# Kernel tuning notes

Hardware: AMD Instinct MI355X
Metric: run time of the kernel (lower is better)

## Reference

```python
import math
import jax, jax.numpy as jnp
import numpy as np

B, N, D = 8, 1024, 1024


def setup_inputs() -> dict:
    key = jax.random.key(0)
    ks = jax.random.split(key, 5)
    scale = 1.0 / math.sqrt(D)  # ~torch Linear init scale
    x = jax.random.normal(ks[0], (B, N, D), jnp.float32)
    Wq = jax.random.uniform(ks[1], (D, D), jnp.float32, -scale, scale)
    Wk = jax.random.uniform(ks[2], (D, D), jnp.float32, -scale, scale)
    Wv = jax.random.uniform(ks[3], (D, D), jnp.float32, -scale, scale)
    Ws = jax.random.uniform(ks[4], (D, 1), jnp.float32, -scale, scale)
    return {"x": x, "Wq": Wq, "Wk": Wk, "Wv": Wv, "Ws": Ws}


def reference(x, Wq, Wk, Wv, Ws):
    # projections
    Q = x @ Wq                      # [B, N, D]
    K = x @ Wk
    V = x @ Wv
    sigma = x @ Ws                  # [B, N, 1]
    sigma = jax.nn.sigmoid(sigma * 5.0) + 1e-5
    sigma = jnp.power(3.0, sigma) - 1.0

    # prior association: Gaussian kernel over |i-j| distances
    idx = jnp.arange(N, dtype=jnp.float32)
    dist = jnp.abs(idx[:, None] - idx[None, :])            # [N, N]
    inv_norm = 1.0 / (jnp.sqrt(2.0 * jnp.pi) * sigma)      # [B, N, 1]
    gaussian = inv_norm * jnp.exp(-0.5 * jnp.square(dist / sigma))  # [B, N, N]
    P = gaussian / gaussian.sum(axis=(1, 2), keepdims=True)

    # series association: softmax over the BATCH dim (dim=0), as in source
    scores = jnp.einsum('bnd,bmd->bnm', Q, K) / math.sqrt(D)  # [B, N, N]
    S = jax.nn.softmax(scores, axis=0)

    # reconstruction
    Z = jnp.einsum('bnm,bmd->bnd', S, V)                     # [B, N, D]
    return Z, P
```

## Files before the change

### kernel.cpp

```cpp
#include <hip/hip_runtime.h>
#include <hip/hip_fp16.h>


typedef __attribute__((ext_vector_type(8))) short bf16x8;
typedef __attribute__((ext_vector_type(4))) float f32x4;
typedef unsigned short ushort_t;

#define DI __device__ __forceinline__

constexpr long NN = 1024L * 1024L;
constexpr long ND = 1024L * 1024L;

DI ushort_t f2bf(float f) {
    unsigned int u = __float_as_uint(f);
    u = u + 0x7fffu + ((u >> 16) & 1u);
    return (ushort_t)(u >> 16);
}
DI ushort_t f2h(float f) {
    __half h = __float2half(f);
    return *(ushort_t*)&h;
}
DI float h2f(ushort_t u) {
    __half h = *(__half*)&u;
    return __half2float(h);
}

template <int OUT_BF16>
DI void g3b_body(const ushort_t* __restrict__ Ab, const ushort_t* __restrict__ Bb,
                 void* __restrict__ Cb, int ldA, int ldB, int ldC,
                 float scale, int bx, int by, ushort_t* lds)
{
    constexpr int BUF   = 24576;
    constexpr int B_OFF = 8192;

    const int tid  = threadIdx.x;
    const int wave = tid >> 6;
    const int lane = tid & 63;
    const int wm   = wave >> 2;
    const int wn   = wave & 3;
    const int gm   = bx * 128;
    const int gn   = by * 256;

    const int srow = tid >> 3;
    const int scol = 8 * ((tid & 7) ^ (srow & 7));
    const int sdst = wave * 512;

    auto stageA = [&](int t, int d, int h) {
        const ushort_t* src = Ab + (long)(gm + h * 64 + srow) * ldA + t * 64 + scol;
        __builtin_amdgcn_global_load_lds(
            (const __attribute__((address_space(1))) void*)src,
            (__attribute__((address_space(3))) void*)(&lds[d * BUF + h * 4096 + sdst]),
            16, 0, 0);
    };
    auto stageB = [&](int t, int d, int h, int j) {
        const ushort_t* src = Bb + (long)(gn + h * 128 + j * 64 + srow) * ldB + t * 64 + scol;
        __builtin_amdgcn_global_load_lds(
            (const __attribute__((address_space(1))) void*)src,
            (__attribute__((address_space(3))) void*)(&lds[d * BUF + B_OFF + h * 8192 + j * 4096 + sdst]),
            16, 0, 0);
    };

    const int arow = wm * 64 + (lane & 15);
    const int brow = wn * 64 + (lane & 15);
    const int cs0 = (((lane >> 4) * 16) ^ ((lane & 7) << 4)) >> 1;
    const int cs1 = ((64 + (lane >> 4) * 16) ^ ((lane & 7) << 4)) >> 1;

    f32x4 acc[4][4];
#pragma unroll
    for (int m = 0; m < 4; ++m)
#pragma unroll
        for (int n = 0; n < 4; ++n) acc[m][n] = (f32x4){0.f, 0.f, 0.f, 0.f};

    stageA(0, 0, 0); stageA(0, 0, 1);
    stageB(0, 0, 0, 0); stageB(0, 0, 0, 1); stageB(0, 0, 1, 0); stageB(0, 0, 1, 1);
    stageA(1, 1, 0); stageA(1, 1, 1);
    stageB(1, 1, 0, 0); stageB(1, 1, 0, 1); stageB(1, 1, 1, 0); stageB(1, 1, 1, 1);
    asm volatile("s_waitcnt vmcnt(6)" ::: "memory");
    __builtin_amdgcn_s_barrier();
    __builtin_amdgcn_sched_barrier(0);

    int cur = 0;
    for (int t = 0; t < 16; ++t) {
        const int nxt = (cur == 0) ? 2 : cur - 1;
        const ushort_t* la = &lds[cur * BUF];
        const ushort_t* lb = &lds[cur * BUF + B_OFF];

        bf16x8 a[2][4], b[2][4];
#pragma unroll
        for (int mi = 0; mi < 4; ++mi) {
            a[0][mi] = *(const bf16x8*)&la[(arow + mi * 16) * 64 + cs0];
            a[1][mi] = *(const bf16x8*)&la[(arow + mi * 16) * 64 + cs1];
        }
#pragma unroll
        for (int ni = 0; ni < 2; ++ni) {
            b[0][ni] = *(const bf16x8*)&lb[(brow + ni * 16) * 64 + cs0];
            b[1][ni] = *(const bf16x8*)&lb[(brow + ni * 16) * 64 + cs1];
        }
        if (t < 14) {
            stageB(t + 2, nxt, 0, 0); stageB(t + 2, nxt, 0, 1);
            stageB(t + 2, nxt, 1, 0); stageB(t + 2, nxt, 1, 1);
        }
        __builtin_amdgcn_s_barrier();
        asm volatile("s_waitcnt lgkmcnt(0)" ::: "memory");
        __builtin_amdgcn_sched_barrier(0);
        __builtin_amdgcn_s_setprio(1);
#pragma unroll
        for (int mi = 0; mi < 4; ++mi)
#pragma unroll
            for (int ni = 0; ni < 2; ++ni) {
                acc[mi][ni] = __builtin_amdgcn_mfma_f32_16x16x32_bf16(a[0][mi], b[0][ni], acc[mi][ni], 0, 0, 0);
                acc[mi][ni] = __builtin_amdgcn_mfma_f32_16x16x32_bf16(a[1][mi], b[1][ni], acc[mi][ni], 0, 0, 0);
            }
        __builtin_amdgcn_s_setprio(0);
        __builtin_amdgcn_s_barrier();
        __builtin_amdgcn_sched_barrier(0);

#pragma unroll
        for (int ni = 2; ni < 4; ++ni) {
            b[0][ni] = *(const bf16x8*)&lb[(brow + ni * 16) * 64 + cs0];
            b[1][ni] = *(const bf16x8*)&lb[(brow + ni * 16) * 64 + cs1];
        }
        if (t < 14) { stageA(t + 2, nxt, 0); stageA(t + 2, nxt, 1); }
        __builtin_amdgcn_s_barrier();
        asm volatile("s_waitcnt lgkmcnt(0)" ::: "memory");
        if (t < 14) asm volatile("s_waitcnt vmcnt(6)" ::: "memory");
        else        asm volatile("s_waitcnt vmcnt(0)" ::: "memory");
        __builtin_amdgcn_sched_barrier(0);
        __builtin_amdgcn_s_setprio(1);
#pragma unroll
        for (int mi = 0; mi < 4; ++mi)
#pragma unroll
            for (int ni = 2; ni < 4; ++ni) {
                acc[mi][ni] = __builtin_amdgcn_mfma_f32_16x16x32_bf16(a[0][mi], b[0][ni], acc[mi][ni], 0, 0, 0);
                acc[mi][ni] = __builtin_amdgcn_mfma_f32_16x16x32_bf16(a[1][mi], b[1][ni], acc[mi][ni], 0, 0, 0);
            }
        __builtin_amdgcn_s_setprio(0);
        __builtin_amdgcn_s_barrier();
        __builtin_amdgcn_sched_barrier(0);

        cur = (cur == 2) ? 0 : cur + 1;
    }

    if (OUT_BF16) {
        ushort_t* el = lds;
#pragma unroll
        for (int mi = 0; mi < 4; ++mi)
#pragma unroll
            for (int ni = 0; ni < 4; ++ni)
#pragma unroll
                for (int r = 0; r < 4; ++r)
                    el[(wm * 64 + mi * 16 + (lane >> 4) * 4 + r) * 256 +
                       wn * 64 + ni * 16 + (lane & 15)] = f2bf(acc[mi][ni][r] * scale);
        __builtin_amdgcn_s_barrier();
        ushort_t* C = (ushort_t*)Cb;
#pragma unroll
        for (int rr = 0; rr < 8; ++rr) {
            const int row = rr * 16 + (tid >> 5);
            const int col = (tid & 31) * 8;
            *(bf16x8*)&C[(long)(gm + row) * ldC + gn + col] =
                *(const bf16x8*)&el[row * 256 + col];
        }
    } else {
        float* el = (float*)lds;
        float* C  = (float*)Cb;
#pragma unroll
        for (int h = 0; h < 2; ++h) {
            if (wm == h) {
#pragma unroll
                for (int mi = 0; mi < 4; ++mi)
#pragma unroll
                    for (int ni = 0; ni < 4; ++ni)
#pragma unroll
                        for (int r = 0; r < 4; ++r)
                            el[(mi * 16 + (lane >> 4) * 4 + r) * 256 +
                               wn * 64 + ni * 16 + (lane & 15)] = acc[mi][ni][r] * scale;
            }
            __builtin_amdgcn_s_barrier();
#pragma unroll
            for (int i = 0; i < 8; ++i) {
                const int cc  = i * 512 + tid;
                const int row = cc >> 6;
                const int c4  = (cc & 63) * 4;
                *(float4*)&C[(long)(gm + h * 64 + row) * ldC + gn + c4] =
                    *(const float4*)&el[row * 256 + c4];
            }
            __builtin_amdgcn_s_barrier();
        }
    }
}

template <int OUT_BF16>
__global__ __launch_bounds__(512, 2)
void gemm3b(const ushort_t* __restrict__ A, const ushort_t* __restrict__ B,
            void* __restrict__ Cout, int ldA, int ldB, int ldC,
            long sA, long sB, long sC, float scale,
            int n0, int n1, int xfirst)
{
    __shared__ ushort_t lds[3 * 24576];
    const int total = gridDim.x;
    const int lin   = blockIdx.x;
    const int swz   = (lin & 7) * (total >> 3) + (lin >> 3);
    const int c0    = swz % n0;
    const int rem   = swz / n0;
    const int c1    = rem % n1;
    const int bz    = rem / n1;
    const int bx    = xfirst ? c0 : c1;
    const int by    = xfirst ? c1 : c0;
    void* Cb = OUT_BF16 ? (void*)((ushort_t*)Cout + (long)bz * sC)
                        : (void*)((float*)Cout + (long)bz * sC);
    g3b_body<OUT_BF16>(A + (long)bz * sA, B + (long)bz * sB, Cb,
                       ldA, ldB, ldC, scale, bx, by, lds);
}

template <int OUT_MODE>
DI void g256_body(const ushort_t* __restrict__ Ab, const ushort_t* __restrict__ Bb,
                  void* __restrict__ Cb, int ldA, int ldB, int ldC,
                  float scale, int bx, int by, ushort_t* ldsp)
{
    constexpr int BUF   = 32768;
    constexpr int B_OFF = 16384;

    const int tid  = threadIdx.x;
    const int wave = tid >> 6;
    const int lane = tid & 63;
    const int wm   = wave >> 2;
    const int wn   = wave & 3;
    const int gm   = bx * 256;
    const int gn   = by * 256;

    const int srow = tid >> 3;
    const int scol = 8 * ((tid & 7) ^ (srow & 7));
    const int sdst = wave * 512;

    auto stage = [&](int t, int d, int op, int h) {
        const ushort_t* g  = op ? Bb : Ab;
        const int       ld = op ? ldB : ldA;
        const int       g0 = (op ? gn : gm) + h * 128;
#pragma unroll
        for (int j = 0; j < 2; ++j) {
            const ushort_t* src = g + (long)(g0 + j * 64 + srow) * ld + t * 64 + scol;
            __builtin_amdgcn_global_load_lds(
                (const __attribute__((address_space(1))) void*)src,
                (__attribute__((address_space(3))) void*)
                    (&ldsp[d * BUF + op * B_OFF + h * 8192 + j * 4096 + sdst]),
                16, 0, 0);
        }
    };

    const int arow = wm * 128 + (lane & 15);
    const int brow = wn * 64 + (lane & 15);
    const int cs0 = (((lane >> 4) * 16) ^ ((lane & 7) << 4)) >> 1;
    const int cs1 = ((64 + (lane >> 4) * 16) ^ ((lane & 7) << 4)) >> 1;

    f32x4 acc[8][4];
#pragma unroll
    for (int m = 0; m < 8; ++m)
#pragma unroll
        for (int n = 0; n < 4; ++n) acc[m][n] = (f32x4){0.f, 0.f, 0.f, 0.f};

    stage(0, 0, 0, 0); stage(0, 0, 0, 1); stage(0, 0, 1, 0); stage(0, 0, 1, 1);
    stage(1, 1, 0, 0); stage(1, 1, 0, 1); stage(1, 1, 1, 0); stage(1, 1, 1, 1);
    asm volatile("s_waitcnt vmcnt(8)" ::: "memory");
    __builtin_amdgcn_s_barrier();
    __builtin_amdgcn_sched_barrier(0);

    bf16x8 a[2][4], b0[2][2], b1[2][2];
#pragma unroll 2
    for (int t = 0; t < 16; ++t) {
        const int cur = t & 1;
        const ushort_t* la = &ldsp[cur * BUF];
        const ushort_t* lb = &ldsp[cur * BUF + B_OFF];

#pragma unroll
        for (int mi = 0; mi < 4; ++mi) {
            a[0][mi] = *(const bf16x8*)&la[(arow + mi * 16) * 64 + cs0];
            a[1][mi] = *(const bf16x8*)&la[(arow + mi * 16) * 64 + cs1];
        }
#pragma unroll
        for (int ni = 0; ni < 2; ++ni) {
            b0[0][ni] = *(const bf16x8*)&lb[(brow + ni * 16) * 64 + cs0];
            b0[1][ni] = *(const bf16x8*)&lb[(brow + ni * 16) * 64 + cs1];
        }
        __builtin_amdgcn_s_barrier();
        asm volatile("s_waitcnt lgkmcnt(0)" ::: "memory");
        __builtin_amdgcn_sched_barrier(0);
        __builtin_amdgcn_s_setprio(1);
#pragma unroll
        for (int mi = 0; mi < 4; ++mi)
#pragma unroll
            for (int ni = 0; ni < 2; ++ni) {
                acc[mi][ni] = __builtin_amdgcn_mfma_f32_16x16x32_bf16(a[0][mi], b0[0][ni], acc[mi][ni], 0, 0, 0);
                acc[mi][ni] = __builtin_amdgcn_mfma_f32_16x16x32_bf16(a[1][mi], b0[1][ni], acc[mi][ni], 0, 0, 0);
            }
        __builtin_amdgcn_s_setprio(0);
        __builtin_amdgcn_s_barrier();
        __builtin_amdgcn_sched_barrier(0);

#pragma unroll
        for (int ni = 0; ni < 2; ++ni) {
            b1[0][ni] = *(const bf16x8*)&lb[(brow + (ni + 2) * 16) * 64 + cs0];
            b1[1][ni] = *(const bf16x8*)&lb[(brow + (ni + 2) * 16) * 64 + cs1];
        }
        __builtin_amdgcn_s_barrier();
        asm volatile("s_waitcnt lgkmcnt(0)" ::: "memory");
        __builtin_amdgcn_sched_barrier(0);
        __builtin_amdgcn_s_setprio(1);
#pragma unroll
        for (int mi = 0; mi < 4; ++mi)
#pragma unroll
            for (int ni = 0; ni < 2; ++ni) {
                acc[mi][ni + 2] = __builtin_amdgcn_mfma_f32_16x16x32_bf16(a[0][mi], b1[0][ni], acc[mi][ni + 2], 0, 0, 0);
                acc[mi][ni + 2] = __builtin_amdgcn_mfma_f32_16x16x32_bf16(a[1][mi], b1[1][ni], acc[mi][ni + 2], 0, 0, 0);
            }
        __builtin_amdgcn_s_setprio(0);
        __builtin_amdgcn_s_barrier();
        __builtin_amdgcn_sched_barrier(0);

#pragma unroll
        for (int mi = 0; mi < 4; ++mi) {
            a[0][mi] = *(const bf16x8*)&la[(arow + (mi + 4) * 16) * 64 + cs0];
            a[1][mi] = *(const bf16x8*)&la[(arow + (mi + 4) * 16) * 64 + cs1];
        }
        if (t < 14) { stage(t + 2, cur, 1, 0); stage(t + 2, cur, 1, 1); }
        __builtin_amdgcn_s_barrier();
        asm volatile("s_waitcnt lgkmcnt(0)" ::: "memory");
        __builtin_amdgcn_sched_barrier(0);
        __builtin_amdgcn_s_setprio(1);
#pragma unroll
        for (int mi = 0; mi < 4; ++mi)
#pragma unroll
            for (int ni = 0; ni < 2; ++ni) {
                acc[mi + 4][ni + 2] = __builtin_amdgcn_mfma_f32_16x16x32_bf16(a[0][mi], b1[0][ni], acc[mi + 4][ni + 2], 0, 0, 0);
                acc[mi + 4][ni + 2] = __builtin_amdgcn_mfma_f32_16x16x32_bf16(a[1][mi], b1[1][ni], acc[mi + 4][ni + 2], 0, 0, 0);
            }
        __builtin_amdgcn_s_setprio(0);
        __builtin_amdgcn_s_barrier();
        __builtin_amdgcn_sched_barrier(0);

        if (t < 14) { stage(t + 2, cur, 0, 0); stage(t + 2, cur, 0, 1); }
        if (t < 14)       asm volatile("s_waitcnt vmcnt(8)" ::: "memory");
        else if (t == 14) asm volatile("s_waitcnt vmcnt(0)" ::: "memory");
        __builtin_amdgcn_sched_barrier(0);
        __builtin_amdgcn_s_setprio(1);
#pragma unroll
        for (int mi = 0; mi < 4; ++mi)
#pragma unroll
            for (int ni = 0; ni < 2; ++ni) {
                acc[mi + 4][ni] = __builtin_amdgcn_mfma_f32_16x16x32_bf16(a[0][mi], b0[0][ni], acc[mi + 4][ni], 0, 0, 0);
                acc[mi + 4][ni] = __builtin_amdgcn_mfma_f32_16x16x32_bf16(a[1][mi], b0[1][ni], acc[mi + 4][ni], 0, 0, 0);
            }
        __builtin_amdgcn_s_setprio(0);
        __builtin_amdgcn_s_barrier();
        __builtin_amdgcn_sched_barrier(0);
    }

    if (OUT_MODE != 0) {
        ushort_t* el = ldsp;
#pragma unroll
        for (int mi = 0; mi < 8; ++mi)
#pragma unroll
            for (int ni = 0; ni < 4; ++ni)
#pragma unroll
                for (int r = 0; r < 4; ++r) {
                    const float v = acc[mi][ni][r] * scale;
                    el[(wm * 128 + mi * 16 + (lane >> 4) * 4 + r) * 256 +
                       wn * 64 + ni * 16 + (lane & 15)] =
                        (OUT_MODE == 1) ? f2bf(v) : f2h(v);
                }
        __builtin_amdgcn_s_barrier();
        ushort_t* C = (ushort_t*)Cb;
#pragma unroll
        for (int i = 0; i < 16; ++i) {
            const int cc  = i * 512 + tid;
            const int row = cc >> 5;
            const int col = (cc & 31) * 8;
            *(bf16x8*)&C[(long)(gm + row) * ldC + gn + col] =
                *(const bf16x8*)&el[row * 256 + col];
        }
    } else {
        float* el = (float*)ldsp;
        float* C  = (float*)Cb;
#pragma unroll
        for (int h = 0; h < 2; ++h) {
            if (wm == h) {
#pragma unroll
                for (int mi = 0; mi < 8; ++mi)
#pragma unroll
                    for (int ni = 0; ni < 4; ++ni)
#pragma unroll
                        for (int r = 0; r < 4; ++r)
                            el[(mi * 16 + (lane >> 4) * 4 + r) * 256 +
                               wn * 64 + ni * 16 + (lane & 15)] = acc[mi][ni][r] * scale;
            }
            __builtin_amdgcn_s_barrier();
#pragma unroll
            for (int i = 0; i < 16; ++i) {
                const int cc  = i * 512 + tid;
                const int row = cc >> 6;
                const int c4  = (cc & 63) * 4;
                *(float4*)&C[(long)(gm + h * 128 + row) * ldC + gn + c4] =
                    *(const float4*)&el[row * 256 + c4];
            }
            __builtin_amdgcn_s_barrier();
        }
    }
}

__global__ __launch_bounds__(512)
void prep_g(const float* __restrict__ x, const float* __restrict__ Ws,
            const float* __restrict__ Wq, const float* __restrict__ Wk,
            const float* __restrict__ Wv,
            ushort_t* __restrict__ xh, float* __restrict__ sigma,
            float* __restrict__ rowsum,
            ushort_t* __restrict__ WvT, ushort_t* __restrict__ G)
{
    __shared__ char smem[20608];
    const int blk = blockIdx.x;
    const int tid = threadIdx.x;

    if (blk < 160) {
        const int wave = tid >> 6, lane = tid & 63;
        for (int row = blk * 8 + wave; row < 8192; row += 1280) {
            const float* xr = x + (long)row * 1024;
            float dot = 0.f;
#pragma unroll
            for (int c = 0; c < 4; ++c) {
                const int i = c * 256 + lane * 4;
                float4 v = *(const float4*)(xr + i);
                float4 w = *(const float4*)(Ws + i);
                dot += v.x * w.x + v.y * w.y + v.z * w.z + v.w * w.w;
                ushort4 o;
                o.x = f2bf(v.x); o.y = f2bf(v.y); o.z = f2bf(v.z); o.w = f2bf(v.w);
                *(ushort4*)(xh + (long)row * 1024 + i) = o;
            }
#pragma unroll
            for (int o = 32; o; o >>= 1) dot += __shfl_down(dot, o);
            float sg;
            if (lane == 0) {
                float s = 1.f / (1.f + __expf(-5.f * dot)) + 1e-5f;
                sg = exp2f(s * 1.5849625007211562f) - 1.f;
            }
            sg = __shfl(sg, 0);
            const int i = row & 1023;
            const float c = -0.5f / (sg * sg);
            float a = 0.f;
            for (int j = lane; j < 1024; j += 64) {
                float d = (float)(i - j);
                a += __expf(c * d * d);
            }
#pragma unroll
            for (int o = 32; o; o >>= 1) a += __shfl_down(a, o);
            if (lane == 0) {
                sigma[row]  = sg;
                rowsum[row] = (0.3989422804014327f / sg) * a;
            }
        }
    } else if (blk < 192) {
        float (*s)[65] = (float(*)[65])smem;
        const int r = tid >> 4, c4 = (tid & 15) * 4;
#pragma unroll
        for (int it = 0; it < 8; ++it) {
            const int tile = (blk - 160) * 8 + it;
            const int tr = (tile >> 4) * 64, tc = (tile & 15) * 64;
#pragma unroll
            for (int rr = r; rr < 64; rr += 32) {
                float4 v = *(const float4*)(Wv + (long)(tr + rr) * 1024 + tc + c4);
                s[rr][c4] = v.x; s[rr][c4 + 1] = v.y; s[rr][c4 + 2] = v.z; s[rr][c4 + 3] = v.w;
            }
            __syncthreads();
#pragma unroll
            for (int rr = r; rr < 64; rr += 32) {
                ushort4 o;
                o.x = f2bf(s[c4][rr]);     o.y = f2bf(s[c4 + 1][rr]);
                o.z = f2bf(s[c4 + 2][rr]); o.w = f2bf(s[c4 + 3][rr]);
                *(ushort4*)(WvT + (long)(tc + rr) * 1024 + tr + c4) = o;
            }
            __syncthreads();
        }
    } else {
        ushort_t* sA = (ushort_t*)smem;
        ushort_t* sB = sA + 5120;
        const int g  = blk - 192;
        const int gm = (g >> 3) * 128, gn = (g & 7) * 128;
        const int wave = tid >> 6, lane = tid & 63;
        const int wm = wave >> 2, wn = wave & 3;
        const int lrow = tid >> 3, lcol = (tid & 7) * 4;
        const float* A0 = Wk + (long)(gm + lrow) * 1024 + lcol;
        const float* A1 = Wk + (long)(gm + 64 + lrow) * 1024 + lcol;
        const float* B0 = Wq + (long)(gn + lrow) * 1024 + lcol;
        const float* B1 = Wq + (long)(gn + 64 + lrow) * 1024 + lcol;

        f32x4 acc[4][2];
#pragma unroll
        for (int m = 0; m < 4; ++m)
#pragma unroll
            for (int n = 0; n < 2; ++n) acc[m][n] = (f32x4){0.f, 0.f, 0.f, 0.f};

        auto wr = [&](float4 a0, float4 a1, float4 b0, float4 b1) {
            ushort4 o;
            o.x = f2bf(a0.x); o.y = f2bf(a0.y); o.z = f2bf(a0.z); o.w = f2bf(a0.w);
            *(ushort4*)&sA[lrow * 40 + lcol] = o;
            o.x = f2bf(a1.x); o.y = f2bf(a1.y); o.z = f2bf(a1.z); o.w = f2bf(a1.w);
            *(ushort4*)&sA[(64 + lrow) * 40 + lcol] = o;
            o.x = f2bf(b0.x); o.y = f2bf(b0.y); o.z = f2bf(b0.z); o.w = f2bf(b0.w);
            *(ushort4*)&sB[lrow * 40 + lcol] = o;
            o.x = f2bf(b1.x); o.y = f2bf(b1.y); o.z = f2bf(b1.z); o.w = f2bf(b1.w);
            *(ushort4*)&sB[(64 + lrow) * 40 + lcol] = o;
        };
        auto mm = [&]() {
            bf16x8 af[4], bfv[2];
#pragma unroll
            for (int mi = 0; mi < 4; ++mi)
                af[mi] = *(const bf16x8*)&sA[(wm * 64 + mi * 16 + (lane & 15)) * 40 + (lane >> 4) * 8];
#pragma unroll
            for (int ni = 0; ni < 2; ++ni)
                bfv[ni] = *(const bf16x8*)&sB[(wn * 32 + ni * 16 + (lane & 15)) * 40 + (lane >> 4) * 8];
#pragma unroll
            for (int mi = 0; mi < 4; ++mi)
#pragma unroll
                for (int ni = 0; ni < 2; ++ni)
                    acc[mi][ni] = __builtin_amdgcn_mfma_f32_16x16x32_bf16(af[mi], bfv[ni], acc[mi][ni], 0, 0, 0);
        };

        float4 a0A = *(const float4*)(A0);      float4 a1A = *(const float4*)(A1);
        float4 b0A = *(const float4*)(B0);      float4 b1A = *(const float4*)(B1);
        float4 a0B = *(const float4*)(A0 + 32); float4 a1B = *(const float4*)(A1 + 32);
        float4 b0B = *(const float4*)(B0 + 32); float4 b1B = *(const float4*)(B1 + 32);

        for (int k0 = 0; k0 < 1024; k0 += 64) {
            wr(a0A, a1A, b0A, b1A);
            if (k0 < 960) {
                a0A = *(const float4*)(A0 + k0 + 64); a1A = *(const float4*)(A1 + k0 + 64);
                b0A = *(const float4*)(B0 + k0 + 64); b1A = *(const float4*)(B1 + k0 + 64);
            }
            __syncthreads();
            mm();
            __syncthreads();
            wr(a0B, a1B, b0B, b1B);
            if (k0 < 928) {
                a0B = *(const float4*)(A0 + k0 + 96); a1B = *(const float4*)(A1 + k0 + 96);
                b0B = *(const float4*)(B0 + k0 + 96); b1B = *(const float4*)(B1 + k0 + 96);
            }
            __syncthreads();
            mm();
            __syncthreads();
        }
#pragma unroll
        for (int mi = 0; mi < 4; ++mi)
#pragma unroll
            for (int ni = 0; ni < 2; ++ni)
#pragma unroll
                for (int r = 0; r < 4; ++r)
                    G[(long)(gm + wm * 64 + mi * 16 + (lane >> 4) * 4 + r) * 1024 +
                      gn + wn * 32 + ni * 16 + (lane & 15)] = f2bf(acc[mi][ni][r]);
    }
}

__global__ __launch_bounds__(512, 2)
void sc_vt(const ushort_t* __restrict__ xqh, const ushort_t* __restrict__ xh,
           ushort_t* __restrict__ scoresH,
           const ushort_t* __restrict__ WvT, ushort_t* __restrict__ VTall)
{
    __shared__ ushort_t lds[2 * 32768];
    const int lin = blockIdx.x;
    if (lin < 128) {
        const int bz = lin & 7;
        const int t  = lin >> 3;
        g256_body<2>(xqh + (long)bz * ND, xh + (long)bz * ND,
                     (void*)(scoresH + (long)bz * NN),
                     1024, 1024, 1024, 0.03125f, t & 3, t >> 2, lds);
    } else {
        const int l  = lin - 128;
        const int l2 = (l & 7) * 16 + (l >> 3);
        g256_body<1>(WvT, xh, (void*)VTall,
                     1024, 1024, 8192, 1.f, l2 & 3, l2 >> 2, lds);
    }
}

__global__ __launch_bounds__(256)
void softmax_prior(const ushort_t* __restrict__ scoresH, ushort_t* __restrict__ S,
                   const float* __restrict__ sigma, const float* __restrict__ rowsum,
                   float* __restrict__ P)
{
    __shared__ float sred[256];
    const int blk = blockIdx.x;
    const int tid = threadIdx.x;
    if (blk < 4096) {
        const long idx = (long)blk * 256 + tid;
        float v[8], m = -1e30f;
#pragma unroll
        for (int b = 0; b < 8; ++b) { v[b] = h2f(scoresH[(long)b * NN + idx]); m = fmaxf(m, v[b]); }
        float sum = 0.f;
#pragma unroll
        for (int b = 0; b < 8; ++b) { v[b] = __expf(v[b] - m); sum += v[b]; }
        const float inv = 1.f / sum;
#pragma unroll
        for (int b = 0; b < 8; ++b) S[(long)b * NN + idx] = f2bf(v[b] * inv);
    } else {
        const int l = blk - 4096;
        const int b = l >> 7;
        float a = rowsum[b * 1024 + tid]       + rowsum[b * 1024 + 256 + tid] +
                  rowsum[b * 1024 + 512 + tid] + rowsum[b * 1024 + 768 + tid];
        sred[tid] = a; __syncthreads();
        for (int o = 128; o; o >>= 1) { if (tid < o) sred[tid] += sred[tid + o]; __syncthreads(); }
        const float bs = sred[0];
        const int r0 = (l & 127) * 8;
#pragma unroll
        for (int it = 0; it < 8; ++it) {
            const int e   = it * 256 + tid;
            const int row = r0 + (e >> 8);
            const int j4  = (e & 255) * 4;
            const float sg  = sigma[(b << 10) + row];
            const float c   = -0.5f / (sg * sg);
            const float inv = 0.3989422804014327f / (sg * bs);
            float4 o;
            float d;
            d = (float)(row - j4);       o.x = inv * __expf(c * d * d);
            d = (float)(row - j4 - 1);   o.y = inv * __expf(c * d * d);
            d = (float)(row - j4 - 2);   o.z = inv * __expf(c * d * d);
            d = (float)(row - j4 - 3);   o.w = inv * __expf(c * d * d);
            *(float4*)&P[(long)b * NN + (long)row * 1024 + j4] = o;
        }
    }
}

extern "C" void kernel_launch(void* const* d_in, const int* in_sizes, int n_in,
                              void* d_out, int out_size, void* d_ws, size_t ws_size,
                              hipStream_t stream)
{
    const float* x  = (const float*)d_in[0];
    const float* Wq = (const float*)d_in[1];
    const float* Wk = (const float*)d_in[2];
    const float* Wv = (const float*)d_in[3];
    const float* Ws = (const float*)d_in[4];
    float* Zout = (float*)d_out;
    float* Pout = Zout + 8 * ND;

    char* base = (char*)d_ws;
    size_t off = 0;
    auto alloc = [&](size_t bytes) {
        void* p = base + off;
        off = (off + bytes + 255) & ~(size_t)255;
        return p;
    };
    ushort_t* xh      = (ushort_t*)alloc(8192L * 1024 * 2);
    ushort_t* G       = (ushort_t*)alloc(NN * 2);
    ushort_t* WvT     = (ushort_t*)alloc(NN * 2);
    ushort_t* xqh     = (ushort_t*)alloc(8192L * 1024 * 2);
    ushort_t* VTall   = (ushort_t*)alloc(1024L * 8192 * 2);
    ushort_t* scoresH = (ushort_t*)alloc(8L * NN * 2);
    float* sigma      = (float*)alloc(8192 * 4);
    float* rowsum     = (float*)alloc(8192 * 4);
    ushort_t* Sh      = xh;

    prep_g<<<256, 512, 0, stream>>>(x, Ws, Wq, Wk, Wv, xh, sigma, rowsum, WvT, G);
    gemm3b<1><<<256, 512, 0, stream>>>(
        xh, G, xqh, 1024, 1024, 1024, 0, 0, 0, 1.f, 4, 64, 0);
    sc_vt<<<256, 512, 0, stream>>>(xqh, xh, scoresH, WvT, VTall);
    softmax_prior<<<5120, 256, 0, stream>>>(scoresH, Sh, sigma, rowsum, Pout);
    gemm3b<0><<<256, 512, 0, stream>>>(
        Sh, VTall, Zout, 1024, 8192, 1024, NN, 1024, ND, 1.f, 8, 4, 1);
}
```

Before: 118.9 us.

## Shrink GEMM tile to 128x128 with double-buffered LDS and more blocks

Replaces the 128x256 triple-buffered GEMM with a 128x128 tile, two LDS buffers, and a unified stage helper. Grid size doubles to 512 blocks and launch bounds allow four blocks per CU. The aim is better occupancy and CU fill for the two 1024-wide GEMMs. The cost is less operand reuse per block, so more global and LDS traffic per FLOP, plus a shallower prefetch pipeline.

```diff
diff --git a/kernel.cpp b/kernel.cpp
--- a/kernel.cpp
+++ b/kernel.cpp
@@ -26,11 +26,11 @@
 }
 
 template <int OUT_BF16>
-DI void g3b_body(const ushort_t* __restrict__ Ab, const ushort_t* __restrict__ Bb,
+DI void g2b_body(const ushort_t* __restrict__ Ab, const ushort_t* __restrict__ Bb,
                  void* __restrict__ Cb, int ldA, int ldB, int ldC,
                  float scale, int bx, int by, ushort_t* lds)
 {
-    constexpr int BUF   = 24576;
+    constexpr int BUF   = 16384;
     constexpr int B_OFF = 8192;
 
     const int tid  = threadIdx.x;
@@ -39,53 +39,48 @@
     const int wm   = wave >> 2;
     const int wn   = wave & 3;
     const int gm   = bx * 128;
-    const int gn   = by * 256;
+    const int gn   = by * 128;
 
     const int srow = tid >> 3;
     const int scol = 8 * ((tid & 7) ^ (srow & 7));
     const int sdst = wave * 512;
 
-    auto stageA = [&](int t, int d, int h) {
-        const ushort_t* src = Ab + (long)(gm + h * 64 + srow) * ldA + t * 64 + scol;
+    auto stage = [&](int t, int d, int op, int h) {
+        const ushort_t* g  = op ? Bb : Ab;
+        const int       ld = op ? ldB : ldA;
+        const int       g0 = (op ? gn : gm) + h * 64;
+        const ushort_t* src = g + (long)(g0 + srow) * ld + t * 64 + scol;
         __builtin_amdgcn_global_load_lds(
             (const __attribute__((address_space(1))) void*)src,
-            (__attribute__((address_space(3))) void*)(&lds[d * BUF + h * 4096 + sdst]),
+            (__attribute__((address_space(3))) void*)
+                (&lds[d * BUF + op * B_OFF + h * 4096 + sdst]),
             16, 0, 0);
     };
-    auto stageB = [&](int t, int d, int h, int j) {
-        const ushort_t* src = Bb + (long)(gn + h * 128 + j * 64 + srow) * ldB + t * 64 + scol;
-        __builtin_amdgcn_global_load_lds(
-            (const __attribute__((address_space(1))) void*)src,
-            (__attribute__((address_space(3))) void*)(&lds[d * BUF + B_OFF + h * 8192 + j * 4096 + sdst]),
-            16, 0, 0);
-    };
 
     const int arow = wm * 64 + (lane & 15);
-    const int brow = wn * 64 + (lane & 15);
+    const int brow = wn * 32 + (lane & 15);
     const int cs0 = (((lane >> 4) * 16) ^ ((lane & 7) << 4)) >> 1;
     const int cs1 = ((64 + (lane >> 4) * 16) ^ ((lane & 7) << 4)) >> 1;
 
-    f32x4 acc[4][4];
+    f32x4 acc[4][2];
 #pragma unroll
     for (int m = 0; m < 4; ++m)
 #pragma unroll
-        for (int n = 0; n < 4; ++n) acc[m][n] = (f32x4){0.f, 0.f, 0.f, 0.f};
-
-    stageA(0, 0, 0); stageA(0, 0, 1);
-    stageB(0, 0, 0, 0); stageB(0, 0, 0, 1); stageB(0, 0, 1, 0); stageB(0, 0, 1, 1);
-    stageA(1, 1, 0); stageA(1, 1, 1);
-    stageB(1, 1, 0, 0); stageB(1, 1, 0, 1); stageB(1, 1, 1, 0); stageB(1, 1, 1, 1);
-    asm volatile("s_waitcnt vmcnt(6)" ::: "memory");
+        for (int n = 0; n < 2; ++n) acc[m][n] = (f32x4){0.f, 0.f, 0.f, 0.f};
+
+    stage(0, 0, 0, 0); stage(0, 0, 0, 1); stage(0, 0, 1, 0); stage(0, 0, 1, 1);
+    stage(1, 1, 0, 0); stage(1, 1, 0, 1); stage(1, 1, 1, 0); stage(1, 1, 1, 1);
+    asm volatile("s_waitcnt vmcnt(4)" ::: "memory");
     __builtin_amdgcn_s_barrier();
     __builtin_amdgcn_sched_barrier(0);
 
-    int cur = 0;
+#pragma unroll 2
     for (int t = 0; t < 16; ++t) {
-        const int nxt = (cur == 0) ? 2 : cur - 1;
+        const int cur = t & 1;
         const ushort_t* la = &lds[cur * BUF];
         const ushort_t* lb = &lds[cur * BUF + B_OFF];
 
-        bf16x8 a[2][4], b[2][4];
+        bf16x8 a[2][4], b[2][2];
 #pragma unroll
         for (int mi = 0; mi < 4; ++mi) {
             a[0][mi] = *(const bf16x8*)&la[(arow + mi * 16) * 64 + cs0];
@@ -96,49 +91,41 @@
             b[0][ni] = *(const bf16x8*)&lb[(brow + ni * 16) * 64 + cs0];
             b[1][ni] = *(const bf16x8*)&lb[(brow + ni * 16) * 64 + cs1];
         }
-        if (t < 14) {
-            stageB(t + 2, nxt, 0, 0); stageB(t + 2, nxt, 0, 1);
-            stageB(t + 2, nxt, 1, 0); stageB(t + 2, nxt, 1, 1);
-        }
         __builtin_amdgcn_s_barrier();
         asm volatile("s_waitcnt lgkmcnt(0)" ::: "memory");
         __builtin_amdgcn_sched_barrier(0);
         __builtin_amdgcn_s_setprio(1);
 #pragma unroll
-        for (int mi = 0; mi < 4; ++mi)
+        for (int mi = 0; mi < 2; ++mi)
 #pragma unroll
             for (int ni = 0; ni < 2; ++ni) {
                 acc[mi][ni] = __builtin_amdgcn_mfma_f32_16x16x32_bf16(a[0][mi], b[0][ni], acc[mi][ni], 0, 0, 0);
                 acc[mi][ni] = __builtin_amdgcn_mfma_f32_16x16x32_bf16(a[1][mi], b[1][ni], acc[mi][ni], 0, 0, 0);
             }
         __builtin_amdgcn_s_setprio(0);
-        __builtin_amdgcn_s_barrier();
-        __builtin_amdgcn_sched_barrier(0);
-
-#pragma unroll
-        for (int ni = 2; ni < 4; ++ni) {
-            b[0][ni] = *(const bf16x8*)&lb[(brow + ni * 16) * 64 + cs0];
-            b[1][ni] = *(const bf16x8*)&lb[(brow + ni * 16) * 64 + cs1];
-        }
-        if (t < 14) { stageA(t + 2, nxt, 0); stageA(t + 2, nxt, 1); }
-        __builtin_amdgcn_s_barrier();
-        asm volatile("s_waitcnt lgkmcnt(0)" ::: "memory");
-        if (t < 14) asm volatile("s_waitcnt vmcnt(6)" ::: "memory");
-        else        asm volatile("s_waitcnt vmcnt(0)" ::: "memory");
+        __builtin_amdgcn_sched_barrier(0);
+        __builtin_amdgcn_s_barrier();
+        __builtin_amdgcn_sched_barrier(0);
+
+        if (t < 14) {
+            stage(t + 2, cur, 0, 0); stage(t + 2, cur, 0, 1);
+            stage(t + 2, cur, 1, 0); stage(t + 2, cur, 1, 1);
+        }
+        if (t < 14)       asm volatile("s_waitcnt vmcnt(4)" ::: "memory");
+        else if (t == 14) asm volatile("s_waitcnt vmcnt(0)" ::: "memory");
         __builtin_amdgcn_sched_barrier(0);
         __builtin_amdgcn_s_setprio(1);
 #pragma unroll
-        for (int mi = 0; mi < 4; ++mi)
-#pragma unroll
-            for (int ni = 2; ni < 4; ++ni) {
+        for (int mi = 2; mi < 4; ++mi)
+#pragma unroll
+            for (int ni = 0; ni < 2; ++ni) {
                 acc[mi][ni] = __builtin_amdgcn_mfma_f32_16x16x32_bf16(a[0][mi], b[0][ni], acc[mi][ni], 0, 0, 0);
                 acc[mi][ni] = __builtin_amdgcn_mfma_f32_16x16x32_bf16(a[1][mi], b[1][ni], acc[mi][ni], 0, 0, 0);
             }
         __builtin_amdgcn_s_setprio(0);
-        __builtin_amdgcn_s_barrier();
-        __builtin_amdgcn_sched_barrier(0);
-
-        cur = (cur == 2) ? 0 : cur + 1;
+        __builtin_amdgcn_sched_barrier(0);
+        __builtin_amdgcn_s_barrier();
+        __builtin_amdgcn_sched_barrier(0);
     }
 
     if (OUT_BF16) {
@@ -146,57 +133,52 @@
 #pragma unroll
         for (int mi = 0; mi < 4; ++mi)
 #pragma unroll
-            for (int ni = 0; ni < 4; ++ni)
+            for (int ni = 0; ni < 2; ++ni)
 #pragma unroll
                 for (int r = 0; r < 4; ++r)
-                    el[(wm * 64 + mi * 16 + (lane >> 4) * 4 + r) * 256 +
-                       wn * 64 + ni * 16 + (lane & 15)] = f2bf(acc[mi][ni][r] * scale);
+                    el[(wm * 64 + mi * 16 + (lane >> 4) * 4 + r) * 128 +
+                       wn * 32 + ni * 16 + (lane & 15)] = f2bf(acc[mi][ni][r] * scale);
         __builtin_amdgcn_s_barrier();
         ushort_t* C = (ushort_t*)Cb;
 #pragma unroll
-        for (int rr = 0; rr < 8; ++rr) {
-            const int row = rr * 16 + (tid >> 5);
-            const int col = (tid & 31) * 8;
+        for (int i = 0; i < 4; ++i) {
+            const int cc  = i * 512 + tid;
+            const int row = cc >> 4;
+            const int col = (cc & 15) * 8;
             *(bf16x8*)&C[(long)(gm + row) * ldC + gn + col] =
-                *(const bf16x8*)&el[row * 256 + col];
+                *(const bf16x8*)&el[row * 128 + col];
         }
     } else {
         float* el = (float*)lds;
         float* C  = (float*)Cb;
 #pragma unroll
-        for (int h = 0; h < 2; ++h) {
-            if (wm == h) {
-#pragma unroll
-                for (int mi = 0; mi < 4; ++mi)
-#pragma unroll
-                    for (int ni = 0; ni < 4; ++ni)
-#pragma unroll
-                        for (int r = 0; r < 4; ++r)
-                            el[(mi * 16 + (lane >> 4) * 4 + r) * 256 +
-                               wn * 64 + ni * 16 + (lane & 15)] = acc[mi][ni][r] * scale;
-            }
-            __builtin_amdgcn_s_barrier();
-#pragma unroll
-            for (int i = 0; i < 8; ++i) {
-                const int cc  = i * 512 + tid;
-                const int row = cc >> 6;
-                const int c4  = (cc & 63) * 4;
-                *(float4*)&C[(long)(gm + h * 64 + row) * ldC + gn + c4] =
-                    *(const float4*)&el[row * 256 + c4];
-            }
-            __builtin_amdgcn_s_barrier();
+        for (int mi = 0; mi < 4; ++mi)
+#pragma unroll
+            for (int ni = 0; ni < 2; ++ni)
+#pragma unroll
+                for (int r = 0; r < 4; ++r)
+                    el[(wm * 64 + mi * 16 + (lane >> 4) * 4 + r) * 128 +
+                       wn * 32 + ni * 16 + (lane & 15)] = acc[mi][ni][r] * scale;
+        __builtin_amdgcn_s_barrier();
+#pragma unroll
+        for (int i = 0; i < 8; ++i) {
+            const int cc  = i * 512 + tid;
+            const int row = cc >> 5;
+            const int c4  = (cc & 31) * 4;
+            *(float4*)&C[(long)(gm + row) * ldC + gn + c4] =
+                *(const float4*)&el[row * 128 + c4];
         }
     }
 }
 
 template <int OUT_BF16>
-__global__ __launch_bounds__(512, 2)
-void gemm3b(const ushort_t* __restrict__ A, const ushort_t* __restrict__ B,
-            void* __restrict__ Cout, int ldA, int ldB, int ldC,
-            long sA, long sB, long sC, float scale,
-            int n0, int n1, int xfirst)
+__global__ __launch_bounds__(512, 4)
+void g2b(const ushort_t* __restrict__ A, const ushort_t* __restrict__ B,
+         void* __restrict__ Cout, int ldA, int ldB, int ldC,
+         long sA, long sB, long sC, float scale,
+         int n0, int n1, int xfirst)
 {
-    __shared__ ushort_t lds[3 * 24576];
+    __shared__ ushort_t lds[2 * 16384];
     const int total = gridDim.x;
     const int lin   = blockIdx.x;
     const int swz   = (lin & 7) * (total >> 3) + (lin >> 3);
@@ -208,7 +190,7 @@
     const int by    = xfirst ? c1 : c0;
     void* Cb = OUT_BF16 ? (void*)((ushort_t*)Cout + (long)bz * sC)
                         : (void*)((float*)Cout + (long)bz * sC);
-    g3b_body<OUT_BF16>(A + (long)bz * sA, B + (long)bz * sB, Cb,
+    g2b_body<OUT_BF16>(A + (long)bz * sA, B + (long)bz * sB, Cb,
                        ldA, ldB, ldC, scale, bx, by, lds);
 }
 
@@ -654,10 +636,10 @@
     ushort_t* Sh      = xh;
 
     prep_g<<<256, 512, 0, stream>>>(x, Ws, Wq, Wk, Wv, xh, sigma, rowsum, WvT, G);
-    gemm3b<1><<<256, 512, 0, stream>>>(
-        xh, G, xqh, 1024, 1024, 1024, 0, 0, 0, 1.f, 4, 64, 0);
+    g2b<1><<<512, 512, 0, stream>>>(
+        xh, G, xqh, 1024, 1024, 1024, 0, 0, 0, 1.f, 8, 64, 0);
     sc_vt<<<256, 512, 0, stream>>>(xqh, xh, scoresH, WvT, VTall);
     softmax_prior<<<5120, 256, 0, stream>>>(scoresH, Sh, sigma, rowsum, Pout);
-    gemm3b<0><<<256, 512, 0, stream>>>(
-        Sh, VTall, Zout, 1024, 8192, 1024, NN, 1024, ND, 1.f, 8, 4, 1);
-}
+    g2b<0><<<512, 512, 0, stream>>>(
+        Sh, VTall, Zout, 1024, 8192, 1024, NN, 1024, ND, 1.f, 8, 8, 1);
+}
```

Result: no change. 117.9 us (-0.8%).
